# Optimization experiments

Measured on AMD Instinct MI355X. Metric: run time of the kernel, lower is better.

## Reference

```python
import jax, jax.numpy as jnp
import numpy as np

B, S, U, M = 4096, 64, 128, 32
ODE_UNFOLDS = 6
EPS = 1e-08

def _uniform(k, shape, lo, hi):
    return jax.random.uniform(k, shape, jnp.float32, lo, hi)

def setup_inputs() -> dict:
    key = jax.random.key(0)
    ks = jax.random.split(key, 16)
    return {
        "inputs": jax.random.normal(ks[0], (B, S), jnp.float32),
        "state": jax.random.normal(ks[1], (B, U), jnp.float32),
        "gleak": _uniform(ks[2], (U,), 0.001, 1.0),
        "vleak": _uniform(ks[3], (U,), -0.2, 0.2),
        "cm": _uniform(ks[4], (U,), 0.4, 0.6),
        "sigma": _uniform(ks[5], (U, U), 3.0, 8.0),
        "mu": _uniform(ks[6], (U, U), 0.3, 0.8),
        "w": _uniform(ks[7], (U, U), 0.001, 1.0),
        "erev": jnp.sign(jax.random.normal(ks[8], (U, U), jnp.float32)),
        "sensory_sigma": _uniform(ks[9], (S, U), 3.0, 8.0),
        "sensory_mu": _uniform(ks[10], (S, U), 0.3, 0.8),
        "sensory_w": _uniform(ks[11], (S, U), 0.001, 1.0),
        "sensory_erev": jnp.sign(jax.random.normal(ks[12], (S, U), jnp.float32)),
        "sparsity_mask": (jax.random.uniform(ks[13], (U, U)) < 0.5).astype(jnp.float32),
        "sensory_sparsity_mask": (jax.random.uniform(ks[14], (S, U)) < 0.5).astype(jnp.float32),
        "input_w": jnp.ones((S,), jnp.float32),
        "input_b": jnp.zeros((S,), jnp.float32),
        "output_w": jnp.ones((M,), jnp.float32),
        "output_b": jnp.zeros((M,), jnp.float32),
    }

def reference(inputs, state, gleak, vleak, cm, sigma, mu, w, erev,
              sensory_sigma, sensory_mu, sensory_w, sensory_erev,
              sparsity_mask, sensory_sparsity_mask,
              input_w, input_b, output_w, output_b):
    # input mapping (affine)
    x = inputs * input_w + input_b                       # [B,S]
    # sensory synapse activation: [B,S,U]
    sens_act = (sensory_w * sensory_sparsity_mask) * jax.nn.sigmoid(
        sensory_sigma * (x[:, :, None] - sensory_mu))
    w_num_sensory = jnp.sum(sens_act * sensory_erev, axis=1)   # [B,U]
    w_den_sensory = jnp.sum(sens_act, axis=1)                  # [B,U]

    wm = w * sparsity_mask                                     # masked weights [U,U]
    wme = wm * erev                                            # weights*erev   [U,U]
    cm_t = cm * ODE_UNFOLDS                                    # cm / (1/unfolds)
    leak = gleak * vleak

    v = state
    for _ in range(ODE_UNFOLDS):
        sig = jax.nn.sigmoid(sigma * (v[:, :, None] - mu))     # [B,U,U] (src,dst)
        w_num = jnp.einsum('bsu,su->bu', sig, wme) + w_num_sensory
        w_den = jnp.einsum('bsu,su->bu', sig, wm) + w_den_sensory
        v = (cm_t * v + leak + w_num) / (cm_t + gleak + w_den + EPS)

    out = v[:, :M] * output_w + output_b                       # motor slice + affine
    return out, v
```

## Files before the change

### kernel.cpp

```cpp
#include <hip/hip_runtime.h>
#include <hip/hip_fp16.h>

typedef unsigned short u16;
typedef unsigned int   u32;

#define B_TOTAL 4096
#define NU      128
#define NS      64
#define NM      32
#define UNFOLDS 6
#define LOG2E   1.44269504088896340736f

__device__ __forceinline__ float bf2f(u16 v) {
  return __uint_as_float(((u32)v) << 16);
}
__device__ __forceinline__ u16 f2bf(float f) {
  u32 x = __float_as_uint(f);
  return (u16)((x + 0x7fffu + ((x >> 16) & 1u)) >> 16);
}

template<bool BF16>
__device__ __forceinline__ float LD(const void* p, int i) {
  if (BF16) return bf2f(((const u16*)p)[i]);
  return ((const float*)p)[i];
}

__device__ __forceinline__ float rdlane(float v, int lane) {
  return __int_as_float(__builtin_amdgcn_readlane(__float_as_int(v), lane));
}

__device__ __forceinline__ u32 pk(float a, float b) {
  __half2 h = __halves2half2(__float2half_rn(a), __float2half_rn(b));
  return __builtin_bit_cast(u32, h);
}
__device__ __forceinline__ float lo2f(u32 h) {
  return __low2float(__builtin_bit_cast(__half2, h));
}
__device__ __forceinline__ float hi2f(u32 h) {
  return __high2float(__builtin_bit_cast(__half2, h));
}

__device__ __forceinline__ void step2i(uint4 a, float va, float vb,
                                       float& na0, float& da0, float& na1, float& da1,
                                       float& nb0, float& db0, float& nb1, float& db1) {
  float ta0 = fmaf(va, lo2f(a.x), lo2f(a.y));
  float ta1 = fmaf(va, hi2f(a.x), hi2f(a.y));
  float tb0 = fmaf(vb, lo2f(a.x), lo2f(a.y));
  float tb1 = fmaf(vb, hi2f(a.x), hi2f(a.y));
  float ea0 = __builtin_amdgcn_exp2f(ta0);
  float ea1 = __builtin_amdgcn_exp2f(ta1);
  float eb0 = __builtin_amdgcn_exp2f(tb0);
  float eb1 = __builtin_amdgcn_exp2f(tb1);
  float pa0 = 1.0f + ea0, pa1 = 1.0f + ea1;
  float pb0 = 1.0f + eb0, pb1 = 1.0f + eb1;
  float ra = __builtin_amdgcn_rcpf(pa0 * pa1);
  float rb = __builtin_amdgcn_rcpf(pb0 * pb1);
  float sa0 = pa1 * ra, sa1 = pa0 * ra;
  float sb0 = pb1 * rb, sb1 = pb0 * rb;
  na0 = fmaf(sa0, lo2f(a.z), na0);  da0 = fmaf(sa0, lo2f(a.w), da0);
  na1 = fmaf(sa1, hi2f(a.z), na1);  da1 = fmaf(sa1, hi2f(a.w), da1);
  nb0 = fmaf(sb0, lo2f(a.z), nb0);  db0 = fmaf(sb0, lo2f(a.w), db0);
  nb1 = fmaf(sb1, hi2f(a.z), nb1);  db1 = fmaf(sb1, hi2f(a.w), db1);
}

template<bool BF16>
__device__ __forceinline__ void body(
    const void* g_in, const void* g_state, const void* g_gleak, const void* g_vleak,
    const void* g_cm, const void* g_sigma, const void* g_mu, const void* g_w,
    const void* g_erev, const void* g_ssig, const void* g_smu, const void* g_sw,
    const void* g_serev, const void* g_mask, const void* g_smask,
    const void* g_iw, const void* g_ib, const void* g_ow, const void* g_ob,
    void* g_out,
    uint4* smR)
{
  const int tid = threadIdx.x;
  const int b0  = blockIdx.x * 16;

  const int r  = tid >> 6;
  const int u0 = tid & 63;
  const int u1 = u0 + 64;
  const int ba = b0 + 2 * r;
  const int bb = ba + 1;

  #pragma unroll 2
  for (int e = tid; e < NS * 64; e += 512) {
    int s = e >> 6, l = e & 63;
    int i0 = s * NU + l, i1 = i0 + 64;
    float sl0 = LD<BF16>(g_ssig, i0) * LOG2E, sl1 = LD<BF16>(g_ssig, i1) * LOG2E;
    float ms0 = LD<BF16>(g_smu, i0) * sl0,    ms1 = LD<BF16>(g_smu, i1) * sl1;
    float w0 = LD<BF16>(g_sw, i0) * LD<BF16>(g_smask, i0) * LD<BF16>(g_serev, i0);
    float w1 = LD<BF16>(g_sw, i1) * LD<BF16>(g_smask, i1) * LD<BF16>(g_serev, i1);
    smR[e] = make_uint4(pk(-sl0, -sl1), pk(ms0, ms1), pk(w0, w1),
                        pk(fabsf(w0), fabsf(w1)));
  }
  __syncthreads();

  float iw = LD<BF16>(g_iw, u0), ib = LD<BF16>(g_ib, u0);
  float xa = LD<BF16>(g_in, ba * NS + u0) * iw + ib;
  float xb = LD<BF16>(g_in, bb * NS + u0) * iw + ib;
  float va0 = LD<BF16>(g_state, ba * NU + u0);
  float va1 = LD<BF16>(g_state, ba * NU + u1);
  float vb0 = LD<BF16>(g_state, bb * NU + u0);
  float vb1 = LD<BF16>(g_state, bb * NU + u1);
  const float gl0 = LD<BF16>(g_gleak, u0), gl1 = LD<BF16>(g_gleak, u1);
  const float lk0 = gl0 * LD<BF16>(g_vleak, u0);
  const float lk1 = gl1 * LD<BF16>(g_vleak, u1);
  const float cm0 = LD<BF16>(g_cm, u0) * (float)UNFOLDS;
  const float cm1 = LD<BF16>(g_cm, u1) * (float)UNFOLDS;

  const uint4* pR = smR + u0;

  float nsa0 = 0.f, dsa0 = 0.f, nsa1 = 0.f, dsa1 = 0.f;
  float nsb0 = 0.f, dsb0 = 0.f, nsb1 = 0.f, dsb1 = 0.f;
  #pragma unroll 8
  for (int s = 0; s < NS; ++s) {
    float xsa = rdlane(xa, s);
    float xsb = rdlane(xb, s);
    uint4 a = pR[s * 64];
    step2i(a, xsa, xsb, nsa0, dsa0, nsa1, dsa1, nsb0, dsb0, nsb1, dsb1);
  }
  __syncthreads();

  #pragma unroll 4
  for (int e = tid; e < NU * 64; e += 512) {
    int j = e >> 6, l = e & 63;
    int i0 = j * NU + l, i1 = i0 + 64;
    float sl0 = LD<BF16>(g_sigma, i0) * LOG2E, sl1 = LD<BF16>(g_sigma, i1) * LOG2E;
    float ms0 = LD<BF16>(g_mu, i0) * sl0,      ms1 = LD<BF16>(g_mu, i1) * sl1;
    float w0 = LD<BF16>(g_w, i0) * LD<BF16>(g_mask, i0) * LD<BF16>(g_erev, i0);
    float w1 = LD<BF16>(g_w, i1) * LD<BF16>(g_mask, i1) * LD<BF16>(g_erev, i1);
    smR[e] = make_uint4(pk(-sl0, -sl1), pk(ms0, ms1), pk(w0, w1),
                        pk(fabsf(w0), fabsf(w1)));
  }
  __syncthreads();

  #pragma unroll 1
  for (int it = 0; it < UNFOLDS; ++it) {
    float na0 = nsa0, da0 = dsa0, na1 = nsa1, da1 = dsa1;
    float nb0 = nsb0, db0 = dsb0, nb1 = nsb1, db1 = dsb1;
    #pragma unroll 8
    for (int j = 0; j < 64; ++j) {
      float vja = rdlane(va0, j);
      float vjb = rdlane(vb0, j);
      uint4 a = pR[j * 64];
      step2i(a, vja, vjb, na0, da0, na1, da1, nb0, db0, nb1, db1);
    }
    #pragma unroll 8
    for (int j = 0; j < 64; ++j) {
      float vja = rdlane(va1, j);
      float vjb = rdlane(vb1, j);
      uint4 a = pR[(j + 64) * 64];
      step2i(a, vja, vjb, na0, da0, na1, da1, nb0, db0, nb1, db1);
    }
    va0 = fmaf(cm0, va0, lk0 + na0) * __builtin_amdgcn_rcpf(cm0 + gl0 + da0 + 1e-8f);
    va1 = fmaf(cm1, va1, lk1 + na1) * __builtin_amdgcn_rcpf(cm1 + gl1 + da1 + 1e-8f);
    vb0 = fmaf(cm0, vb0, lk0 + nb0) * __builtin_amdgcn_rcpf(cm0 + gl0 + db0 + 1e-8f);
    vb1 = fmaf(cm1, vb1, lk1 + nb1) * __builtin_amdgcn_rcpf(cm1 + gl1 + db1 + 1e-8f);
  }

  if (BF16) {
    u16* om = (u16*)g_out;
    u16* ov = om + B_TOTAL * NM;
    ov[ba * NU + u0] = f2bf(va0);
    ov[ba * NU + u1] = f2bf(va1);
    ov[bb * NU + u0] = f2bf(vb0);
    ov[bb * NU + u1] = f2bf(vb1);
    if (u0 < NM) {
      float ow = LD<true>(g_ow, u0), ob = LD<true>(g_ob, u0);
      om[ba * NM + u0] = f2bf(fmaf(va0, ow, ob));
      om[bb * NM + u0] = f2bf(fmaf(vb0, ow, ob));
    }
  } else {
    float* om = (float*)g_out;
    float* ov = om + B_TOTAL * NM;
    ov[ba * NU + u0] = va0;
    ov[ba * NU + u1] = va1;
    ov[bb * NU + u0] = vb0;
    ov[bb * NU + u1] = vb1;
    if (u0 < NM) {
      float ow = LD<false>(g_ow, u0), ob = LD<false>(g_ob, u0);
      om[ba * NM + u0] = fmaf(va0, ow, ob);
      om[bb * NM + u0] = fmaf(vb0, ow, ob);
    }
  }
}

__global__ __launch_bounds__(512, 2) void ltc_kernel(
    const void* g_in, const void* g_state, const void* g_gleak, const void* g_vleak,
    const void* g_cm, const void* g_sigma, const void* g_mu, const void* g_w,
    const void* g_erev, const void* g_ssig, const void* g_smu, const void* g_sw,
    const void* g_serev, const void* g_mask, const void* g_smask,
    const void* g_iw, const void* g_ib, const void* g_ow, const void* g_ob,
    void* g_out)
{
  __shared__ uint4 smR[NU * 64];

  const u16* sg = (const u16*)g_sigma;
  int cnt = 0;
  #pragma unroll
  for (int i = 0; i < 32; ++i) {
    float f = bf2f(sg[2 * i]);
    cnt += (f >= 2.0f && f <= 16.0f) ? 1 : 0;
  }
  if (cnt >= 24)
    body<true >(g_in, g_state, g_gleak, g_vleak, g_cm, g_sigma, g_mu, g_w, g_erev,
                g_ssig, g_smu, g_sw, g_serev, g_mask, g_smask,
                g_iw, g_ib, g_ow, g_ob, g_out, smR);
  else
    body<false>(g_in, g_state, g_gleak, g_vleak, g_cm, g_sigma, g_mu, g_w, g_erev,
                g_ssig, g_smu, g_sw, g_serev, g_mask, g_smask,
                g_iw, g_ib, g_ow, g_ob, g_out, smR);
}

extern "C" void kernel_launch(void* const* d_in, const int* in_sizes, int n_in,
                              void* d_out, int out_size, void* d_ws, size_t ws_size,
                              hipStream_t stream) {
  (void)in_sizes; (void)n_in; (void)out_size; (void)d_ws; (void)ws_size;
  dim3 grid(B_TOTAL / 16);
  dim3 block(512);
  hipLaunchKernelGGL(ltc_kernel, grid, block, 0, stream,
                     d_in[0], d_in[1], d_in[2], d_in[3], d_in[4],
                     d_in[5], d_in[6], d_in[7], d_in[8],
                     d_in[9], d_in[10], d_in[11], d_in[12],
                     d_in[13], d_in[14], d_in[15], d_in[16],
                     d_in[17], d_in[18], d_out);
}
```

Before: 206.5 us.

## Replace half of sigmoid evaluations with shared-memory lookup table

Adds a 4096-entry sigmoid table in LDS, covering the range [-16,16) at a step of 1/128. For one of each pair of synapses, the sigmoid is now read from the table via a clamped index instead of computed with exp2 and rcp. The other synapse still uses exp2 and rcp, and the a/b batch rows now share a single reciprocal. The packed layout changes to (slope, offset) pairs per synapse. The aim is to balance transcendental-unit work against LDS reads, at the cost of quantization error, extra LDS bank traffic and 16KB more shared memory per block, which may lower occupancy.

```diff
diff --git a/kernel.cpp b/kernel.cpp
--- a/kernel.cpp
+++ b/kernel.cpp
@@ -40,27 +40,27 @@
   return __high2float(__builtin_bit_cast(__half2, h));
 }
 
-__device__ __forceinline__ void step2i(uint4 a, float va, float vb,
+__device__ __forceinline__ void step2t(uint4 a, float va, float vb,
+                                       const float* __restrict__ sigTab,
                                        float& na0, float& da0, float& na1, float& da1,
                                        float& nb0, float& db0, float& nb1, float& db1) {
-  float ta0 = fmaf(va, lo2f(a.x), lo2f(a.y));
-  float ta1 = fmaf(va, hi2f(a.x), hi2f(a.y));
-  float tb0 = fmaf(vb, lo2f(a.x), lo2f(a.y));
-  float tb1 = fmaf(vb, hi2f(a.x), hi2f(a.y));
-  float ea0 = __builtin_amdgcn_exp2f(ta0);
-  float ea1 = __builtin_amdgcn_exp2f(ta1);
-  float eb0 = __builtin_amdgcn_exp2f(tb0);
-  float eb1 = __builtin_amdgcn_exp2f(tb1);
-  float pa0 = 1.0f + ea0, pa1 = 1.0f + ea1;
-  float pb0 = 1.0f + eb0, pb1 = 1.0f + eb1;
-  float ra = __builtin_amdgcn_rcpf(pa0 * pa1);
-  float rb = __builtin_amdgcn_rcpf(pb0 * pb1);
-  float sa0 = pa1 * ra, sa1 = pa0 * ra;
-  float sb0 = pb1 * rb, sb1 = pb0 * rb;
-  na0 = fmaf(sa0, lo2f(a.z), na0);  da0 = fmaf(sa0, lo2f(a.w), da0);
-  na1 = fmaf(sa1, hi2f(a.z), na1);  da1 = fmaf(sa1, hi2f(a.w), da1);
-  nb0 = fmaf(sb0, lo2f(a.z), nb0);  db0 = fmaf(sb0, lo2f(a.w), db0);
-  nb1 = fmaf(sb1, hi2f(a.z), nb1);  db1 = fmaf(sb1, hi2f(a.w), db1);
+  float ta = fmaf(va, lo2f(a.y), hi2f(a.y));
+  float tb = fmaf(vb, lo2f(a.y), hi2f(a.y));
+  float ea = __builtin_amdgcn_exp2f(ta);
+  float eb = __builtin_amdgcn_exp2f(tb);
+  float pa = 1.0f + ea, pb = 1.0f + eb;
+  float rr = __builtin_amdgcn_rcpf(pa * pb);
+  float sa = pb * rr, sb = pa * rr;
+  na1 = fmaf(sa, hi2f(a.z), na1);  da1 = fmaf(sa, hi2f(a.w), da1);
+  nb1 = fmaf(sb, hi2f(a.z), nb1);  db1 = fmaf(sb, hi2f(a.w), db1);
+  float t0a = fmaf(va, lo2f(a.x), hi2f(a.x));
+  float t0b = fmaf(vb, lo2f(a.x), hi2f(a.x));
+  float fa = __builtin_amdgcn_fmed3f(fmaf(t0a, 128.0f, 2048.5f), 0.0f, 4095.0f);
+  float fb = __builtin_amdgcn_fmed3f(fmaf(t0b, 128.0f, 2048.5f), 0.0f, 4095.0f);
+  float s0a = sigTab[(u32)fa];
+  float s0b = sigTab[(u32)fb];
+  na0 = fmaf(s0a, lo2f(a.z), na0);  da0 = fmaf(s0a, lo2f(a.w), da0);
+  nb0 = fmaf(s0b, lo2f(a.z), nb0);  db0 = fmaf(s0b, lo2f(a.w), db0);
 }
 
 template<bool BF16>
@@ -71,7 +71,7 @@
     const void* g_serev, const void* g_mask, const void* g_smask,
     const void* g_iw, const void* g_ib, const void* g_ow, const void* g_ob,
     void* g_out,
-    uint4* smR)
+    uint4* smR, float* sigTab)
 {
   const int tid = threadIdx.x;
   const int b0  = blockIdx.x * 16;
@@ -81,6 +81,11 @@
   const int u1 = u0 + 64;
   const int ba = b0 + 2 * r;
   const int bb = ba + 1;
+
+  for (int i = tid; i < 4096; i += 512) {
+    float t = (float)(i - 2048) * (1.0f / 128.0f);
+    sigTab[i] = __builtin_amdgcn_rcpf(1.0f + __builtin_amdgcn_exp2f(t));
+  }
 
   #pragma unroll 2
   for (int e = tid; e < NS * 64; e += 512) {
@@ -90,7 +95,7 @@
     float ms0 = LD<BF16>(g_smu, i0) * sl0,    ms1 = LD<BF16>(g_smu, i1) * sl1;
     float w0 = LD<BF16>(g_sw, i0) * LD<BF16>(g_smask, i0) * LD<BF16>(g_serev, i0);
     float w1 = LD<BF16>(g_sw, i1) * LD<BF16>(g_smask, i1) * LD<BF16>(g_serev, i1);
-    smR[e] = make_uint4(pk(-sl0, -sl1), pk(ms0, ms1), pk(w0, w1),
+    smR[e] = make_uint4(pk(-sl0, ms0), pk(-sl1, ms1), pk(w0, w1),
                         pk(fabsf(w0), fabsf(w1)));
   }
   __syncthreads();
@@ -117,7 +122,8 @@
     float xsa = rdlane(xa, s);
     float xsb = rdlane(xb, s);
     uint4 a = pR[s * 64];
-    step2i(a, xsa, xsb, nsa0, dsa0, nsa1, dsa1, nsb0, dsb0, nsb1, dsb1);
+    step2t(a, xsa, xsb, sigTab,
+           nsa0, dsa0, nsa1, dsa1, nsb0, dsb0, nsb1, dsb1);
   }
   __syncthreads();
 
@@ -129,7 +135,7 @@
     float ms0 = LD<BF16>(g_mu, i0) * sl0,      ms1 = LD<BF16>(g_mu, i1) * sl1;
     float w0 = LD<BF16>(g_w, i0) * LD<BF16>(g_mask, i0) * LD<BF16>(g_erev, i0);
     float w1 = LD<BF16>(g_w, i1) * LD<BF16>(g_mask, i1) * LD<BF16>(g_erev, i1);
-    smR[e] = make_uint4(pk(-sl0, -sl1), pk(ms0, ms1), pk(w0, w1),
+    smR[e] = make_uint4(pk(-sl0, ms0), pk(-sl1, ms1), pk(w0, w1),
                         pk(fabsf(w0), fabsf(w1)));
   }
   __syncthreads();
@@ -143,14 +149,16 @@
       float vja = rdlane(va0, j);
       float vjb = rdlane(vb0, j);
       uint4 a = pR[j * 64];
-      step2i(a, vja, vjb, na0, da0, na1, da1, nb0, db0, nb1, db1);
+      step2t(a, vja, vjb, sigTab,
+             na0, da0, na1, da1, nb0, db0, nb1, db1);
     }
     #pragma unroll 8
     for (int j = 0; j < 64; ++j) {
       float vja = rdlane(va1, j);
       float vjb = rdlane(vb1, j);
       uint4 a = pR[(j + 64) * 64];
-      step2i(a, vja, vjb, na0, da0, na1, da1, nb0, db0, nb1, db1);
+      step2t(a, vja, vjb, sigTab,
+             na0, da0, na1, da1, nb0, db0, nb1, db1);
     }
     va0 = fmaf(cm0, va0, lk0 + na0) * __builtin_amdgcn_rcpf(cm0 + gl0 + da0 + 1e-8f);
     va1 = fmaf(cm1, va1, lk1 + na1) * __builtin_amdgcn_rcpf(cm1 + gl1 + da1 + 1e-8f);
@@ -194,6 +202,7 @@
     void* g_out)
 {
   __shared__ uint4 smR[NU * 64];
+  __shared__ float sigTab[4096];
 
   const u16* sg = (const u16*)g_sigma;
   int cnt = 0;
@@ -205,11 +214,11 @@
   if (cnt >= 24)
     body<true >(g_in, g_state, g_gleak, g_vleak, g_cm, g_sigma, g_mu, g_w, g_erev,
                 g_ssig, g_smu, g_sw, g_serev, g_mask, g_smask,
-                g_iw, g_ib, g_ow, g_ob, g_out, smR);
+                g_iw, g_ib, g_ow, g_ob, g_out, smR, sigTab);
   else
     body<false>(g_in, g_state, g_gleak, g_vleak, g_cm, g_sigma, g_mu, g_w, g_erev,
                 g_ssig, g_smu, g_sw, g_serev, g_mask, g_smask,
-                g_iw, g_ib, g_ow, g_ob, g_out, smR);
+                g_iw, g_ib, g_ow, g_ob, g_out, smR, sigTab);
 }
 
 extern "C" void kernel_launch(void* const* d_in, const int* in_sizes, int n_in,
```

After: 207.5 us. No clear change (+0.5%).
